# Optimization experiments

Measured on AMD Instinct MI355X. Metric: run time of the kernel, lower is better.

## Reference

```python
import jax, jax.numpy as jnp
import numpy as np

B = 32768
DIM = 768          # emb dim
NA = 1024          # outer n_anchors
K = 8              # n_comp (= n_patches P in relays)
PD = 16            # patch_dim
RD = K * PD        # relay_dim = 128
L = 2              # n_layers (relays)
RA = 16            # anchors per patch inside RelayLayer
NPH = 3            # n_phases
TD = NPH * RA      # tri_dim = 48
H = 64             # pw_hidden
MAG_MIN, MAG_MAX = 0.1, 5.0


def _nrm(x, eps=1e-12):
    return x / jnp.maximum(jnp.linalg.norm(x, axis=-1, keepdims=True), eps)


def _ln(x, g, b, eps=1e-5):
    mu = jnp.mean(x, axis=-1, keepdims=True)
    var = jnp.mean(jnp.square(x - mu), axis=-1, keepdims=True)
    return (x - mu) * jax.lax.rsqrt(var + eps) * g + b


def setup_inputs() -> dict:
    key = jax.random.key(0)
    ks = jax.random.split(key, 16)
    xav = lambda k, shp, fan_in, fan_out: jax.random.normal(k, shp, jnp.float32) * np.sqrt(2.0 / (fan_in + fan_out))
    home = _nrm(jax.random.normal(ks[3], (L, K, RA, PD), jnp.float32))
    anchors = _nrm(home + 0.05 * jax.random.normal(ks[4], (L, K, RA, PD), jnp.float32))
    return {
        'emb': jax.random.normal(ks[0], (B, DIM), jnp.float32),
        'triangulation': jax.random.normal(ks[1], (B, NA), jnp.float32),
        'raw_magnitude': jax.random.uniform(ks[2], (B, 1), jnp.float32),
        'emb_w': xav(ks[5], (DIM, RD // 2), DIM, RD // 2), 'emb_b': jnp.zeros((RD // 2,), jnp.float32),
        'tri_w': xav(ks[6], (NA, RD // 4), NA, RD // 4), 'tri_b': jnp.zeros((RD // 4,), jnp.float32),
        'ctx_w': xav(ks[7], (RD // 2 + RD // 4 + 1, RD), RD // 2 + RD // 4 + 1, RD), 'ctx_b': jnp.zeros((RD,), jnp.float32),
        'home': home, 'anchors': anchors,
        'pw_w1': xav(ks[8], (L, K, TD, H), TD, H), 'pw_b1': jnp.zeros((L, K, H), jnp.float32),
        'pw_w2': xav(ks[9], (L, K, H, PD), H, PD), 'pw_b2': jnp.zeros((L, K, PD), jnp.float32),
        'pwn_g': jnp.ones((L, PD), jnp.float32), 'pwn_b': jnp.zeros((L, PD), jnp.float32),
        'gates': jnp.full((L, K), -3.0, jnp.float32),
        'norm_g': jnp.ones((L, RD), jnp.float32), 'norm_b': jnp.zeros((L, RD), jnp.float32),
        'head_w1': xav(ks[10], (K, PD, PD // 2), PD, PD // 2), 'head_b1': jnp.zeros((K, PD // 2), jnp.float32),
        'head_w2': xav(ks[11], (K, PD // 2, 1), PD // 2, 1), 'head_b2': jnp.zeros((K, 1), jnp.float32),
        'stats_bias': jnp.zeros((K,), jnp.float32),
    }


def _relay(x, home, anchors, w1, b1, w2, b2, pg, pb, gates, ng, nb):
    Bb = x.shape[0]
    patches = _ln(x, ng, nb).reshape(Bb, K, PD)          # [B,P,d]
    pn = _nrm(patches)
    h = _nrm(home)                                       # [P,A,d]
    c = _nrm(anchors)
    cosw = jnp.clip(jnp.sum(h * c, axis=-1), -1 + 1e-7, 1 - 1e-7)
    omega = jnp.arccos(cosw)[..., None]                  # [P,A,1]
    so = jnp.maximum(jnp.sin(omega), 1e-7)
    tris = []
    for t in (0.0, 1.0 / 3.0, 2.0 / 3.0):
        at = _nrm((jnp.sin((1.0 - t) * omega) * h + jnp.sin(t * omega) * c) / so)
        tris.append(1.0 - jnp.einsum('bpd,pad->bpa', pn, at))
    tri = jnp.concatenate(tris, axis=-1)                 # [B,P,3A]
    hh = jax.nn.gelu(jnp.einsum('bpt,pth->bph', tri, w1) + b1, approximate=False)
    pw = _ln(jnp.einsum('bph,phd->bpd', hh, w2) + b2, pg, pb)
    g = jax.nn.sigmoid(gates)[None, :, None]             # [1,P,1]
    return x + (g * pw + (1.0 - g) * patches).reshape(Bb, -1)


def reference(emb, triangulation, raw_magnitude, emb_w, emb_b, tri_w, tri_b, ctx_w, ctx_b,
              home, anchors, pw_w1, pw_b1, pw_w2, pw_b2, pwn_g, pwn_b, gates, norm_g, norm_b,
              head_w1, head_b1, head_w2, head_b2, stats_bias):
    ctx = jnp.concatenate([emb @ emb_w + emb_b, triangulation @ tri_w + tri_b, raw_magnitude], axis=-1)
    x = ctx @ ctx_w + ctx_b                              # [B, RD]
    for l in range(L):
        x = _relay(x, home[l], anchors[l], pw_w1[l], pw_b1[l], pw_w2[l], pw_b2[l],
                   pwn_g[l], pwn_b[l], gates[l], norm_g[l], norm_b[l])
    patches = x.reshape(-1, K, PD)
    h1 = jax.nn.gelu(jnp.einsum('bkd,kdh->bkh', patches, head_w1) + head_b1, approximate=False)
    mc_raw = (jnp.einsum('bkh,kho->bko', h1, head_w2) + head_b2)[..., 0]   # [B,K]
    mc = MAG_MIN + (MAG_MAX - MAG_MIN) * jax.nn.sigmoid(mc_raw + stats_bias)
    mag = jnp.repeat(mc, NA // K, axis=-1)               # [B, NA]
    return (mag, mc)
```

## Files before the change

### kernel.cpp

```cpp
#include <hip/hip_runtime.h>
#include <hip/hip_bf16.h>
#include <math.h>

#define BTOT 32768

typedef float f32x4 __attribute__((ext_vector_type(4)));
typedef __bf16 v8bf __attribute__((ext_vector_type(8)));

__device__ float g_x[BTOT * 128];
__device__ float g_M[2 * 8 * 16 * 64];
__device__ float g_b1p[2 * 8 * 64];
__device__ __align__(16) unsigned short g_wf[1792 * 128];
__device__ float g_beff[128];
__device__ float g_wr[128];

__device__ __forceinline__ float gelu_f(float v) {
    return 0.5f * v * (1.0f + erff(v * 0.70710678118654752f));
}

__device__ __forceinline__ unsigned short f2bf_rne(float x) {
    unsigned u = __float_as_uint(x);
    u += 0x7fffu + ((u >> 16) & 1u);
    return (unsigned short)(u >> 16);
}

#define GLOAD16(gp, lp)                                                        \
    __builtin_amdgcn_global_load_lds(                                          \
        (const __attribute__((address_space(1))) void*)(gp),                   \
        (__attribute__((address_space(3))) void*)(lp), 16, 0, 0)

__global__ __launch_bounds__(64) void k_pre(const float* __restrict__ home,
                                            const float* __restrict__ anchors,
                                            const float* __restrict__ pw_w1,
                                            const float* __restrict__ pw_b1) {
    __shared__ float s_AT[48 * 16];
    const int lp = blockIdx.x;
    const int tid = threadIdx.x;
    if (tid < 48) {
        const int t = tid >> 4, a = tid & 15;
        const float* hp = home + (lp * 16 + a) * 16;
        const float* cp = anchors + (lp * 16 + a) * 16;
        float h[16], c[16], nh = 0.f, nc = 0.f;
#pragma unroll
        for (int i = 0; i < 16; ++i) {
            h[i] = hp[i]; nh = fmaf(h[i], h[i], nh);
            c[i] = cp[i]; nc = fmaf(c[i], c[i], nc);
        }
        const float ih = 1.f / fmaxf(sqrtf(nh), 1e-12f);
        const float ic = 1.f / fmaxf(sqrtf(nc), 1e-12f);
        float cw = 0.f;
#pragma unroll
        for (int i = 0; i < 16; ++i) { h[i] *= ih; c[i] *= ic; cw = fmaf(h[i], c[i], cw); }
        cw = fminf(fmaxf(cw, -1.f + 1e-7f), 1.f - 1e-7f);
        const float om = acosf(cw);
        const float so = fmaxf(sinf(om), 1e-7f);
        const float tt = (float)t * (1.f / 3.f);
        const float s1 = sinf((1.f - tt) * om), s2 = sinf(tt * om);
        float v[16], nv = 0.f;
#pragma unroll
        for (int i = 0; i < 16; ++i) { v[i] = (s1 * h[i] + s2 * c[i]) / so; nv = fmaf(v[i], v[i], nv); }
        const float iv = 1.f / fmaxf(sqrtf(nv), 1e-12f);
#pragma unroll
        for (int i = 0; i < 16; ++i) s_AT[tid * 16 + i] = v[i] * iv;
    }
    __syncthreads();
    const int h = tid;
    const float* w1 = pw_w1 + lp * 48 * 64;
    float b = pw_b1[lp * 64 + h];
    float m[16];
#pragma unroll
    for (int d = 0; d < 16; ++d) m[d] = 0.f;
    for (int j = 0; j < 48; ++j) {
        const float w = w1[j * 64 + h];
        b += w;
#pragma unroll
        for (int d = 0; d < 16; ++d) m[d] = fmaf(s_AT[j * 16 + d], w, m[d]);
    }
    g_b1p[lp * 64 + h] = b;
#pragma unroll
    for (int d = 0; d < 16; ++d) g_M[(lp * 16 + d) * 64 + h] = m[d];
}

__global__ __launch_bounds__(256) void k_fold(const float* __restrict__ emb_w,
                                              const float* __restrict__ tri_w,
                                              const float* __restrict__ ctx_w,
                                              const float* __restrict__ ctx_b,
                                              const float* __restrict__ emb_b,
                                              const float* __restrict__ tri_b) {
    if (blockIdx.x == 56) {
        const int n = threadIdx.x;
        if (n < 128) {
            float b = ctx_b[n];
            for (int c = 0; c < 64; ++c) b = fmaf(emb_b[c], ctx_w[c * 128 + n], b);
            for (int c = 0; c < 32; ++c) b = fmaf(tri_b[c], ctx_w[(64 + c) * 128 + n], b);
            g_beff[n] = b;
            g_wr[n] = ctx_w[96 * 128 + n];
        }
        return;
    }
    __shared__ float sctx[97 * 128];
    for (int q = threadIdx.x; q < 3104; q += 256)
        *(float4*)&sctx[q * 4] = *(const float4*)&ctx_w[q * 4];
    __syncthreads();
    const int kt = blockIdx.x;
    const int kr = threadIdx.x >> 3;
    const int n0 = (threadIdx.x & 7) * 16;
    const int k = kt * 32 + kr;
    float acc[16];
#pragma unroll
    for (int j = 0; j < 16; ++j) acc[j] = 0.f;
    if (k < 768) {
        const float* wrow = emb_w + k * 64;
        for (int c = 0; c < 64; ++c) {
            const float a = wrow[c];
            const float* cx = &sctx[c * 128 + n0];
#pragma unroll
            for (int j = 0; j < 16; ++j) acc[j] = fmaf(a, cx[j], acc[j]);
        }
    } else {
        const float* wrow = tri_w + (k - 768) * 32;
        for (int c = 0; c < 32; ++c) {
            const float a = wrow[c];
            const float* cx = &sctx[(64 + c) * 128 + n0];
#pragma unroll
            for (int j = 0; j < 16; ++j) acc[j] = fmaf(a, cx[j], acc[j]);
        }
    }
    const int nt = threadIdx.x & 7;
    const int lanehi = (kr >> 3) << 4;
    const int j8 = kr & 7;
#pragma unroll
    for (int q = 0; q < 16; ++q) {
        const int lane = lanehi | q;
        g_wf[((kt * 8 + nt) * 64 + lane) * 8 + j8] = f2bf_rne(acc[q]);
    }
}

__global__ __launch_bounds__(256) void k_front_mfma(const float* __restrict__ emb,
                                                    const float* __restrict__ tri,
                                                    const float* __restrict__ rm) {
    __shared__ __align__(16) char lds[65536];
    const int tid = threadIdx.x;
    const int lane = tid & 63, w = tid >> 6;
    const int row0 = blockIdx.x * 64;
    const int arow = lane & 15, kgrp = lane >> 4;

    f32x4 acc[8];
#pragma unroll
    for (int nt = 0; nt < 8; ++nt) {
        f32x4 z = {0.f, 0.f, 0.f, 0.f};
        acc[nt] = z;
    }

#define STAGE(kc, buf) {                                                       \
        char* AbBase_ = lds + (buf) * 16384 + w * 4096;           \
        char* BbBase_ = lds + 32768 + (buf) * 16384 + w * 4096;                \
        const char* gB_ = (const char*)g_wf + (size_t)(kc) * 16384             \
                          + w * 4096 + lane * 16;                              \
        _Pragma("unroll")                                                      \
        for (int i = 0; i < 4; ++i) GLOAD16(gB_ + i * 1024, BbBase_ + i * 1024); \
        _Pragma("unroll")                                                      \
        for (int i = 0; i < 4; ++i) {                                          \
            const int r_ = i * 4 + (lane >> 4);                                \
            const int grow_ = row0 + w * 16 + r_;                              \
            const int colb_ = ((lane & 15) * 16) ^ (r_ << 4);                  \
            const char* gA_ = ((kc) < 12)                                      \
                ? (const char*)(emb + (size_t)grow_ * 768 + (kc) * 64) + colb_ \
                : (const char*)(tri + (size_t)grow_ * 1024 + ((kc) - 12) * 64) + colb_; \
            GLOAD16(gA_, AbBase_ + i * 1024);                                  \
        }                                                                      \
    }

#define COMPUTE(buf) {                                                         \
        const char* Ar_ = lds + (buf) * 16384 + (w * 16 + arow) * 256;         \
        const char* Br_ = lds + 32768 + (buf) * 16384 + lane * 16;             \
        const int msk_ = arow << 4;                                            \
        _Pragma("unroll")                                                      \
        for (int h = 0; h < 2; ++h) {                                          \
            const int c0_ = h * 128 + kgrp * 32;                               \
            const float4 f0_ = *(const float4*)(Ar_ + (c0_ ^ msk_));           \
            const float4 f1_ = *(const float4*)(Ar_ + ((c0_ + 16) ^ msk_));    \
            v8bf a_;                                                           \
            a_[0] = (__bf16)f0_.x; a_[1] = (__bf16)f0_.y;                      \
            a_[2] = (__bf16)f0_.z; a_[3] = (__bf16)f0_.w;                      \
            a_[4] = (__bf16)f1_.x; a_[5] = (__bf16)f1_.y;                      \
            a_[6] = (__bf16)f1_.z; a_[7] = (__bf16)f1_.w;                      \
            const char* bp_ = Br_ + h * 8192;                                  \
            _Pragma("unroll")                                                  \
            for (int nt = 0; nt < 8; ++nt) {                                   \
                const v8bf b_ = *(const v8bf*)(bp_ + nt * 1024);               \
                acc[nt] = __builtin_amdgcn_mfma_f32_16x16x32_bf16(a_, b_, acc[nt], 0, 0, 0); \
            }                                                                  \
        }                                                                      \
    }

    STAGE(0, 0);
    __syncthreads();
    int buf = 0;
    for (int kc = 0; kc < 28; ++kc) {
        if (kc < 27) STAGE(kc + 1, buf ^ 1);
        COMPUTE(buf);
        __syncthreads();
        buf ^= 1;
    }
#undef STAGE
#undef COMPUTE

    const int rowb = row0 + w * 16 + kgrp * 4;
    const f32x4 rv = *(const f32x4*)&rm[rowb];
#pragma unroll
    for (int nt = 0; nt < 8; ++nt) {
        const int col = nt * 16 + arow;
        const float be = g_beff[col];
        const float wv = g_wr[col];
#pragma unroll
        for (int rr = 0; rr < 4; ++rr) {
            g_x[(size_t)(rowb + rr) * 128 + col] = acc[nt][rr] + rv[rr] * wv + be;
        }
    }
}

__global__ __launch_bounds__(256) void k_relay(
    const float* __restrict__ pw_w2, const float* __restrict__ pw_b2,
    const float* __restrict__ pwn_g, const float* __restrict__ pwn_b,
    const float* __restrict__ gates, const float* __restrict__ norm_g,
    const float* __restrict__ norm_b, const float* __restrict__ head_w1,
    const float* __restrict__ head_b1, const float* __restrict__ head_w2,
    const float* __restrict__ head_b2, const float* __restrict__ stats_bias,
    float* __restrict__ out) {
    __shared__ __align__(16) float s_M[8 * 1028];
    __shared__ __align__(16) float s_w2[8 * 1028];
    __shared__ __align__(16) float s_b1p[8 * 68];
    __shared__ __align__(16) float s_hw1[8 * 132];
    __shared__ float s_hb1[64], s_hw2[64], s_hcb[8];
    __shared__ float s_mc[64 * 8];
    const int tid = threadIdx.x;
    const int pr = tid >> 3, p = tid & 7;
    const int rowA = blockIdx.x * 64 + pr * 2;

    {
        const int e = tid * 4, pp = e >> 7, rem = e & 127;
        *(float4*)&s_hw1[pp * 132 + rem] = *(const float4*)&head_w1[e];
    }
    if (tid < 64) { s_hb1[tid] = head_b1[tid]; s_hw2[tid] = head_w2[tid]; }
    if (tid < 8) s_hcb[tid] = head_b2[tid] + stats_bias[tid];

    float xA[16], xB[16];
    {
        const float* xp = g_x + (size_t)rowA * 128 + p * 16;
#pragma unroll
        for (int i = 0; i < 4; ++i) {
            *(float4*)&xA[i * 4] = *(const float4*)&xp[i * 4];
            *(float4*)&xB[i * 4] = *(const float4*)&xp[128 + i * 4];
        }
    }

    for (int l = 0; l < 2; ++l) {
        if (l) __syncthreads();
        for (int q = tid; q < 2048; q += 256) {
            const int e = q * 4, pp = e >> 10, rem = e & 1023;
            *(float4*)&s_M[pp * 1028 + rem] = *(const float4*)&g_M[l * 8192 + e];
            *(float4*)&s_w2[pp * 1028 + rem] = *(const float4*)&pw_w2[l * 8192 + e];
        }
        if (tid < 128) {
            const int e = tid * 4, pp = e >> 6, rem = e & 63;
            *(float4*)&s_b1p[pp * 68 + rem] = *(const float4*)&g_b1p[l * 512 + e];
        }
        __syncthreads();

        float sA = 0.f, qA = 0.f, sB = 0.f, qB = 0.f;
#pragma unroll
        for (int i = 0; i < 16; ++i) {
            sA += xA[i]; qA = fmaf(xA[i], xA[i], qA);
            sB += xB[i]; qB = fmaf(xB[i], xB[i], qB);
        }
#pragma unroll
        for (int m = 1; m < 8; m <<= 1) {
            sA += __shfl_xor(sA, m, 64); qA += __shfl_xor(qA, m, 64);
            sB += __shfl_xor(sB, m, 64); qB += __shfl_xor(qB, m, 64);
        }
        const float muA = sA * (1.f / 128.f);
        const float rsA = rsqrtf(fmaxf(qA * (1.f / 128.f) - muA * muA, 0.f) + 1e-5f);
        const float muB = sB * (1.f / 128.f);
        const float rsB = rsqrtf(fmaxf(qB * (1.f / 128.f) - muB * muB, 0.f) + 1e-5f);
        float paA[16], paB[16], nA = 0.f, nB = 0.f;
#pragma unroll
        for (int i = 0; i < 16; ++i) {
            const float gg = norm_g[l * 128 + p * 16 + i];
            const float bb = norm_b[l * 128 + p * 16 + i];
            const float vA = (xA[i] - muA) * rsA * gg + bb;
            const float vB = (xB[i] - muB) * rsB * gg + bb;
            paA[i] = vA; nA = fmaf(vA, vA, nA);
            paB[i] = vB; nB = fmaf(vB, vB, nB);
        }
        const float invA = 1.f / fmaxf(sqrtf(nA), 1e-12f);
        const float invB = 1.f / fmaxf(sqrtf(nB), 1e-12f);

        float pwA[16], pwB[16];
#pragma unroll
        for (int i = 0; i < 16; ++i) {
            const float b2 = pw_b2[(l * 8 + p) * 16 + i];
            pwA[i] = b2; pwB[i] = b2;
        }
        const float* Mp = &s_M[p * 1028];
        const float* W2p = &s_w2[p * 1028];
        const float* Bp = &s_b1p[p * 68];
        for (int h4 = 0; h4 < 16; ++h4) {
            float bq[4];
            *(float4*)bq = *(const float4*)&Bp[h4 * 4];
            float aA[4] = {0.f, 0.f, 0.f, 0.f};
            float aB[4] = {0.f, 0.f, 0.f, 0.f};
#pragma unroll
            for (int d = 0; d < 16; ++d) {
                float m4[4];
                *(float4*)m4 = *(const float4*)&Mp[d * 64 + h4 * 4];
#pragma unroll
                for (int j = 0; j < 4; ++j) {
                    aA[j] = fmaf(paA[d], m4[j], aA[j]);
                    aB[j] = fmaf(paB[d], m4[j], aB[j]);
                }
            }
#pragma unroll
            for (int j = 0; j < 4; ++j) {
                const float gA = gelu_f(bq[j] - invA * aA[j]);
                const float gB = gelu_f(bq[j] - invB * aB[j]);
                float w[16];
#pragma unroll
                for (int u = 0; u < 4; ++u)
                    *(float4*)&w[u * 4] = *(const float4*)&W2p[(h4 * 4 + j) * 16 + u * 4];
#pragma unroll
                for (int u = 0; u < 16; ++u) {
                    pwA[u] = fmaf(gA, w[u], pwA[u]);
                    pwB[u] = fmaf(gB, w[u], pwB[u]);
                }
            }
        }
        float s2A = 0.f, q2A = 0.f, s2B = 0.f, q2B = 0.f;
#pragma unroll
        for (int i = 0; i < 16; ++i) {
            s2A += pwA[i]; q2A = fmaf(pwA[i], pwA[i], q2A);
            s2B += pwB[i]; q2B = fmaf(pwB[i], pwB[i], q2B);
        }
        const float mu2A = s2A * (1.f / 16.f);
        const float rs2A = rsqrtf(fmaxf(q2A * (1.f / 16.f) - mu2A * mu2A, 0.f) + 1e-5f);
        const float mu2B = s2B * (1.f / 16.f);
        const float rs2B = rsqrtf(fmaxf(q2B * (1.f / 16.f) - mu2B * mu2B, 0.f) + 1e-5f);
        const float gate = 1.f / (1.f + expf(-gates[l * 8 + p]));
#pragma unroll
        for (int i = 0; i < 16; ++i) {
            const float pg = pwn_g[l * 16 + i], pb = pwn_b[l * 16 + i];
            const float vA = (pwA[i] - mu2A) * rs2A * pg + pb;
            const float vB = (pwB[i] - mu2B) * rs2B * pg + pb;
            xA[i] = xA[i] + gate * vA + (1.f - gate) * paA[i];
            xB[i] = xB[i] + gate * vB + (1.f - gate) * paB[i];
        }
    }

    float accmA = s_hcb[p], accmB = accmA;
#pragma unroll
    for (int j = 0; j < 8; ++j) {
        float aA = s_hb1[p * 8 + j], aB = aA;
#pragma unroll
        for (int d = 0; d < 16; ++d) {
            const float w = s_hw1[p * 132 + d * 8 + j];
            aA = fmaf(xA[d], w, aA);
            aB = fmaf(xB[d], w, aB);
        }
        const float w2h = s_hw2[p * 8 + j];
        accmA = fmaf(gelu_f(aA), w2h, accmA);
        accmB = fmaf(gelu_f(aB), w2h, accmB);
    }
    const float mcA = 0.1f + 4.9f / (1.f + expf(-accmA));
    const float mcB = 0.1f + 4.9f / (1.f + expf(-accmB));
    s_mc[(pr * 2) * 8 + p] = mcA;
    s_mc[(pr * 2 + 1) * 8 + p] = mcB;
    out[(size_t)33554432 + (size_t)rowA * 8 + p] = mcA;
    out[(size_t)33554432 + (size_t)(rowA + 1) * 8 + p] = mcB;
    __syncthreads();

    const size_t base = (size_t)blockIdx.x * 64 * 1024;
#pragma unroll
    for (int it = 0; it < 64; ++it) {
        const int idx = it * 256 + tid;
        const int rr = idx >> 8, c4 = idx & 255;
        const float v = s_mc[rr * 8 + (c4 >> 5)];
        const float4 vv = make_float4(v, v, v, v);
        *(float4*)&out[base + rr * 1024 + c4 * 4] = vv;
    }
}

extern "C" void kernel_launch(void* const* d_in, const int* in_sizes, int n_in,
                              void* d_out, int out_size, void* d_ws, size_t ws_size,
                              hipStream_t stream) {
    (void)in_sizes; (void)n_in; (void)d_ws; (void)ws_size; (void)out_size;
    const float* emb = (const float*)d_in[0];
    const float* tria = (const float*)d_in[1];
    const float* rm = (const float*)d_in[2];
    const float* emb_w = (const float*)d_in[3];
    const float* emb_b = (const float*)d_in[4];
    const float* tri_w = (const float*)d_in[5];
    const float* tri_b = (const float*)d_in[6];
    const float* ctx_w = (const float*)d_in[7];
    const float* ctx_b = (const float*)d_in[8];
    const float* home = (const float*)d_in[9];
    const float* anch = (const float*)d_in[10];
    const float* pw_w1 = (const float*)d_in[11];
    const float* pw_b1 = (const float*)d_in[12];
    const float* pw_w2 = (const float*)d_in[13];
    const float* pw_b2 = (const float*)d_in[14];
    const float* pwn_g = (const float*)d_in[15];
    const float* pwn_b = (const float*)d_in[16];
    const float* gates = (const float*)d_in[17];
    const float* norm_g = (const float*)d_in[18];
    const float* norm_b = (const float*)d_in[19];
    const float* hw1 = (const float*)d_in[20];
    const float* hb1 = (const float*)d_in[21];
    const float* hw2 = (const float*)d_in[22];
    const float* hb2 = (const float*)d_in[23];
    const float* sb = (const float*)d_in[24];
    float* out = (float*)d_out;

    k_pre<<<16, 64, 0, stream>>>(home, anch, pw_w1, pw_b1);
    k_fold<<<57, 256, 0, stream>>>(emb_w, tri_w, ctx_w, ctx_b, emb_b, tri_b);
    k_front_mfma<<<512, 256, 0, stream>>>(emb, tria, rm);
    k_relay<<<512, 256, 0, stream>>>(pw_w2, pw_b2, pwn_g, pwn_b, gates, norm_g, norm_b,
                                     hw1, hb1, hw2, hb2, sb, out);
}
```

Baseline: 176.4 us.

## Load A operand directly to registers and triple-buffer B in LDS

The front GEMM kernel no longer stages the fp32 activation tiles (emb/tri) through LDS. Each lane now loads its A fragment straight from global memory into registers, three stages deep. The bf16 weight tiles go into a three-slot LDS ring, waited on with a manual vmcnt and raw s_barrier instead of __syncthreads double buffering. This cuts LDS traffic and footprint and deepens prefetch to hide global latency. In exchange the global A loads are less coalesced, register pressure rises, and tail iterations issue redundant clamped loads.

New measurement: 178.4 us. About the same (+1.1%).

```diff
diff --git a/kernel.cpp b/kernel.cpp
--- a/kernel.cpp
+++ b/kernel.cpp
@@ -139,7 +139,7 @@
 __global__ __launch_bounds__(256) void k_front_mfma(const float* __restrict__ emb,
                                                     const float* __restrict__ tri,
                                                     const float* __restrict__ rm) {
-    __shared__ __align__(16) char lds[65536];
+    __shared__ __align__(16) char lds[49152];
     const int tid = threadIdx.x;
     const int lane = tid & 63, w = tid >> 6;
     const int row0 = blockIdx.x * 64;
@@ -152,34 +152,34 @@
         acc[nt] = z;
     }
 
-#define STAGE(kc, buf) {                                                       \
-        char* AbBase_ = lds + (buf) * 16384 + w * 4096;           \
-        char* BbBase_ = lds + 32768 + (buf) * 16384 + w * 4096;                \
-        const char* gB_ = (const char*)g_wf + (size_t)(kc) * 16384             \
+    const float* embp = emb + (size_t)(row0 + w * 16 + arow) * 768 + kgrp * 8;
+    const float* trip = tri + (size_t)(row0 + w * 16 + arow) * 1024 + kgrp * 8;
+
+    float4 A0[4], A1[4], A2[4];
+
+#define STAGE_B(kk, BUF) {                                                     \
+        const int k2_ = (kk) < 27 ? (kk) : 27;                                 \
+        const char* gB_ = (const char*)g_wf + (size_t)k2_ * 16384              \
                           + w * 4096 + lane * 16;                              \
+        char* Bb_ = lds + (BUF) * 16384 + w * 4096;               \
         _Pragma("unroll")                                                      \
-        for (int i = 0; i < 4; ++i) GLOAD16(gB_ + i * 1024, BbBase_ + i * 1024); \
-        _Pragma("unroll")                                                      \
-        for (int i = 0; i < 4; ++i) {                                          \
-            const int r_ = i * 4 + (lane >> 4);                                \
-            const int grow_ = row0 + w * 16 + r_;                              \
-            const int colb_ = ((lane & 15) * 16) ^ (r_ << 4);                  \
-            const char* gA_ = ((kc) < 12)                                      \
-                ? (const char*)(emb + (size_t)grow_ * 768 + (kc) * 64) + colb_ \
-                : (const char*)(tri + (size_t)grow_ * 1024 + ((kc) - 12) * 64) + colb_; \
-            GLOAD16(gA_, AbBase_ + i * 1024);                                  \
-        }                                                                      \
-    }
-
-#define COMPUTE(buf) {                                                         \
-        const char* Ar_ = lds + (buf) * 16384 + (w * 16 + arow) * 256;         \
-        const char* Br_ = lds + 32768 + (buf) * 16384 + lane * 16;             \
-        const int msk_ = arow << 4;                                            \
+        for (int i = 0; i < 4; ++i) GLOAD16(gB_ + i * 1024, Bb_ + i * 1024);   \
+    }
+
+#define ALOAD(kk, S) {                                                         \
+        const int k2_ = (kk) < 27 ? (kk) : 27;                                 \
+        const float* ab_ = (k2_ < 12) ? (embp + k2_ * 64) : (trip + (k2_ - 12) * 64); \
+        S[0] = *(const float4*)(ab_);                                          \
+        S[1] = *(const float4*)(ab_ + 4);                                      \
+        S[2] = *(const float4*)(ab_ + 32);                                     \
+        S[3] = *(const float4*)(ab_ + 36);                                     \
+    }
+
+#define COMPUTE(BUF, S) {                                                      \
+        const char* Br_ = lds + (BUF) * 16384 + lane * 16;                     \
         _Pragma("unroll")                                                      \
         for (int h = 0; h < 2; ++h) {                                          \
-            const int c0_ = h * 128 + kgrp * 32;                               \
-            const float4 f0_ = *(const float4*)(Ar_ + (c0_ ^ msk_));           \
-            const float4 f1_ = *(const float4*)(Ar_ + ((c0_ + 16) ^ msk_));    \
+            const float4 f0_ = S[h * 2], f1_ = S[h * 2 + 1];                   \
             v8bf a_;                                                           \
             a_[0] = (__bf16)f0_.x; a_[1] = (__bf16)f0_.y;                      \
             a_[2] = (__bf16)f0_.z; a_[3] = (__bf16)f0_.w;                      \
@@ -194,17 +194,30 @@
         }                                                                      \
     }
 
-    STAGE(0, 0);
-    __syncthreads();
-    int buf = 0;
-    for (int kc = 0; kc < 28; ++kc) {
-        if (kc < 27) STAGE(kc + 1, buf ^ 1);
-        COMPUTE(buf);
-        __syncthreads();
-        buf ^= 1;
-    }
-#undef STAGE
+#define BODY(kk, I0, I2, S0, S2) {                                             \
+        STAGE_B((kk) + 2, I2);                                                 \
+        ALOAD((kk) + 2, S2);                                                   \
+        asm volatile("s_waitcnt vmcnt(16)" ::: "memory");                      \
+        __builtin_amdgcn_s_barrier();                                          \
+        COMPUTE(I0, S0);                                                       \
+        __builtin_amdgcn_s_barrier();                                          \
+    }
+
+    STAGE_B(0, 0); ALOAD(0, A0);
+    STAGE_B(1, 1); ALOAD(1, A1);
+
+    for (int t = 0; t < 9; ++t) {
+        const int k = t * 3;
+        BODY(k,     0, 2, A0, A2);
+        BODY(k + 1, 1, 0, A1, A0);
+        BODY(k + 2, 2, 1, A2, A1);
+    }
+    BODY(27, 0, 2, A0, A2);
+    asm volatile("s_waitcnt vmcnt(0)" ::: "memory");
+#undef STAGE_B
+#undef ALOAD
 #undef COMPUTE
+#undef BODY
 
     const int rowb = row0 + w * 16 + kgrp * 4;
     const f32x4 rv = *(const f32x4*)&rm[rowb];
```
